# Kernel optimization log

Hardware: AMD Instinct MI355X
Metric: run time of the kernel (lower is better)

Reference implementation:

```python
import jax, jax.numpy as jnp
import numpy as np

MAXDISP = 48
GROUP = 40


def setup_inputs() -> dict:
    key = jax.random.key(0)
    k1, k2 = jax.random.split(key)
    left_feature = jax.random.normal(k1, (2, 320, 128, 240), dtype=jnp.float32)
    right_feature = jax.random.normal(k2, (2, 320, 128, 240), dtype=jnp.float32)
    return {"left_feature": left_feature, "right_feature": right_feature}


def reference(left_feature, right_feature):
    # Group-wise correlation cost volume (norm=False path of GwcVolume).
    b, c, h, w = left_feature.shape
    g = GROUP
    cpg = c // g  # channels per group
    lf = left_feature.reshape(b, g, cpg, h, w)
    rf = right_feature.reshape(b, g, cpg, h, w)
    slices = []
    for i in range(MAXDISP):  # static loop over disparities
        if i > 0:
            # correlate left[..., i:] with right[..., :-i], mean over cpg
            cost = (lf[..., i:] * rf[..., : w - i]).mean(axis=2)  # [b,g,h,w-i]
            cost = jnp.pad(cost, ((0, 0), (0, 0), (0, 0), (i, 0)))  # zeros for x < d
        else:
            cost = (lf * rf).mean(axis=2)  # [b,g,h,w]
        slices.append(cost)
    # volume: [b, group, maxdisp, h, w]
    return jnp.stack(slices, axis=2)
```

## Files before the change

### kernel.cpp

```cpp
#include <hip/hip_runtime.h>

constexpr int B = 2, C = 320, H = 128, W = 240;
constexpr int G = 40, CPG = 8, MAXD = 48;
constexpr int HW = H * W;
constexpr int NROW = B * G * H;
constexpr int ROWS_PER_BLOCK = 8;
constexpr int W4 = W / 4;

typedef float f32x4 __attribute__((ext_vector_type(4)));

typedef const __attribute__((address_space(1))) void g_void;
typedef __attribute__((address_space(3))) void lds_void;

__global__ __launch_bounds__(512) void gwc_volume_kernel(
    const float* __restrict__ left, const float* __restrict__ right,
    float* __restrict__ out)
{
    const int tid  = threadIdx.x;
    const int wv   = tid >> 6;
    const int lane = tid & 63;
    const int row  = blockIdx.x * ROWS_PER_BLOCK + wv;

    const int h  = row % H;
    const int bg = row / H;
    const int g  = bg % G;
    const int b  = bg / G;

    __shared__ f32x4 sR4[ROWS_PER_BLOCK][CPG * W4];

    const size_t in_base = ((size_t)(b * C + g * CPG) * H + h) * (size_t)W;

    const int t = lane;
    const bool active = (t < W4);

    f32x4 Lv[CPG];
    if (active) {
        #pragma unroll
        for (int k = 0; k < CPG; ++k)
            Lv[k] = __builtin_nontemporal_load(
                reinterpret_cast<const f32x4*>(left + in_base + (size_t)k * HW + 4 * t));
    }

    #pragma unroll
    for (int i = 0; i < 8; ++i) {
        const int j = i * 64 + lane;
        if (j < CPG * W4) {
            const int k  = j / W4;
            const int x4 = j - k * W4;
            const float* src = right + in_base + (size_t)k * HW + 4 * x4;
            char* dst = (char*)&sR4[wv][0] + (size_t)i * 1024;
            __builtin_amdgcn_global_load_lds((g_void*)src, (lds_void*)dst, 16, 0, 0);
        }
    }

    asm volatile("s_waitcnt vmcnt(0)" ::: "memory");
    __builtin_amdgcn_sched_barrier(0);

    const f32x4* sr = &sR4[wv][0];
    float* outp = out + (((size_t)(b * G + g) * MAXD) * H + h) * (size_t)W + 4 * t;

    #pragma unroll 2
    for (int dg = 0; dg < MAXD / 4; ++dg) {
        __builtin_amdgcn_s_barrier();

        float acc[4][4];
        #pragma unroll
        for (int dd = 0; dd < 4; ++dd)
            #pragma unroll
            for (int xx = 0; xx < 4; ++xx) acc[dd][xx] = 0.f;

        if (active && t >= dg) {
            #pragma unroll
            for (int k = 0; k < CPG; ++k) {
                const int base = k * W4 + (t - dg);
                const f32x4 hi = sr[base];
                f32x4 lo;
                if (t > dg) lo = sr[base - 1];
                else        lo = (f32x4){0.f, 0.f, 0.f, 0.f};
                float win[8];
                win[0] = lo.x; win[1] = lo.y; win[2] = lo.z; win[3] = lo.w;
                win[4] = hi.x; win[5] = hi.y; win[6] = hi.z; win[7] = hi.w;
                #pragma unroll
                for (int dd = 0; dd < 4; ++dd)
                    #pragma unroll
                    for (int xx = 0; xx < 4; ++xx)
                        acc[dd][xx] += Lv[k][xx] * win[4 + xx - dd];
            }
        }

        if (active) {
            #pragma unroll
            for (int dd = 0; dd < 4; ++dd) {
                f32x4 o;
                o.x = acc[dd][0] * 0.125f;
                o.y = acc[dd][1] * 0.125f;
                o.z = acc[dd][2] * 0.125f;
                o.w = acc[dd][3] * 0.125f;
                __builtin_nontemporal_store(
                    o, reinterpret_cast<f32x4*>(outp + (size_t)(dg * 4 + dd) * HW));
            }
        }
    }
}

extern "C" void kernel_launch(void* const* d_in, const int* in_sizes, int n_in,
                              void* d_out, int out_size, void* d_ws, size_t ws_size,
                              hipStream_t stream) {
    const float* left  = (const float*)d_in[0];
    const float* right = (const float*)d_in[1];
    float* out = (float*)d_out;

    dim3 grid(NROW / ROWS_PER_BLOCK);
    dim3 block(512);
    hipLaunchKernelGGL(gwc_volume_kernel, grid, block, 0, stream,
                       left, right, out);
}
```

Before: 120.7 us.

## Stage output tiles through LDS so block writes contiguous 8-row chunks

Each wave now writes its per-disparity results into a shared staging buffer, and the whole block then stores contiguous spans covering 8 consecutive rows (7680 bytes) per disparity plane. Before, each wave stored its own row segment, with 4 lanes idle. The aim is better write coalescing and full use of all threads for the output stores, which dominate traffic. In exchange there are two block barriers per phase, extra LDS round trips, and the loop is no longer unrolled.

```diff
diff --git a/kernel.cpp b/kernel.cpp
--- a/kernel.cpp
+++ b/kernel.cpp
@@ -22,11 +22,13 @@
     const int row  = blockIdx.x * ROWS_PER_BLOCK + wv;
 
     const int h  = row % H;
+    const int h0 = h - wv;
     const int bg = row / H;
     const int g  = bg % G;
     const int b  = bg / G;
 
     __shared__ f32x4 sR4[ROWS_PER_BLOCK][CPG * W4];
+    __shared__ f32x4 wb[2][ROWS_PER_BLOCK][W4];
 
     const size_t in_base = ((size_t)(b * C + g * CPG) * H + h) * (size_t)W;
 
@@ -57,12 +59,11 @@
     __builtin_amdgcn_sched_barrier(0);
 
     const f32x4* sr = &sR4[wv][0];
-    float* outp = out + (((size_t)(b * G + g) * MAXD) * H + h) * (size_t)W + 4 * t;
+    const f32x4* wbflat = &wb[0][0][0];
+    const size_t chunk00 = ((size_t)bg * MAXD * H + h0) * (size_t)W;
 
-    #pragma unroll 2
+    #pragma unroll 1
     for (int dg = 0; dg < MAXD / 4; ++dg) {
-        __builtin_amdgcn_s_barrier();
-
         float acc[4][4];
         #pragma unroll
         for (int dd = 0; dd < 4; ++dd)
@@ -88,17 +89,45 @@
             }
         }
 
-        if (active) {
-            #pragma unroll
-            for (int dd = 0; dd < 4; ++dd) {
-                f32x4 o;
-                o.x = acc[dd][0] * 0.125f;
-                o.y = acc[dd][1] * 0.125f;
-                o.z = acc[dd][2] * 0.125f;
-                o.w = acc[dd][3] * 0.125f;
+        #pragma unroll
+        for (int phase = 0; phase < 2; ++phase) {
+            if (active) {
+                #pragma unroll
+                for (int ddl = 0; ddl < 2; ++ddl) {
+                    const int dd = phase * 2 + ddl;
+                    f32x4 o;
+                    o.x = acc[dd][0] * 0.125f;
+                    o.y = acc[dd][1] * 0.125f;
+                    o.z = acc[dd][2] * 0.125f;
+                    o.w = acc[dd][3] * 0.125f;
+                    wb[ddl][wv][t] = o;
+                }
+            }
+            asm volatile("s_waitcnt lgkmcnt(0)" ::: "memory");
+            __builtin_amdgcn_s_barrier();
+            __builtin_amdgcn_sched_barrier(0);
+
+            const int d_base = dg * 4 + phase * 2;
+            const size_t cbase = chunk00 + (size_t)d_base * HW;
+            {
+                const int f   = tid;
+                const int ddl = f / 480;
+                const int rem = f - ddl * 480;
+                const f32x4 v = wbflat[f];
                 __builtin_nontemporal_store(
-                    o, reinterpret_cast<f32x4*>(outp + (size_t)(dg * 4 + dd) * HW));
+                    v, reinterpret_cast<f32x4*>(out + cbase + (size_t)ddl * HW + 4 * rem));
             }
+            if (tid < 960 - 512) {
+                const int f   = tid + 512;
+                const int rem = f - 480;
+                const f32x4 v = wbflat[f];
+                __builtin_nontemporal_store(
+                    v, reinterpret_cast<f32x4*>(out + cbase + (size_t)HW + 4 * rem));
+            }
+
+            asm volatile("s_waitcnt lgkmcnt(0)" ::: "memory");
+            __builtin_amdgcn_s_barrier();
+            __builtin_amdgcn_sched_barrier(0);
         }
     }
 }
```

New measurement: 117.7 us. -2.5%, faster.
